# Optimization experiments

Measured on AMD Instinct MI355X. Metric: run time of the kernel, lower is better.

Reference implementation:

```python
import jax, jax.numpy as jnp
import numpy as np

N, DEG, D, L = 20000, 32, 128, 2
EPS = 1e-7
MAX_TANH_ARG = 1.0 - 1e-5


def _logmap0(x, sqrt_c):
    # Poincare ball log map at the origin: artanh(sqrt(c)||x||) * x / (sqrt(c)||x||)
    norm = jnp.maximum(jnp.linalg.norm(x, axis=-1, keepdims=True), EPS)
    arg = jnp.minimum(sqrt_c * norm, MAX_TANH_ARG)
    return jnp.arctanh(arg) * x / (sqrt_c * norm)


def _expmap0(v, sqrt_c):
    # Poincare ball exp map at the origin: tanh(sqrt(c)||v||) * v / (sqrt(c)||v||)
    norm = jnp.maximum(jnp.linalg.norm(v, axis=-1, keepdims=True), EPS)
    return jnp.tanh(sqrt_c * norm) * v / (sqrt_c * norm)


def setup_inputs() -> dict:
    key = jax.random.key(0)
    ks = jax.random.split(key, 7)
    neighbors = jax.random.randint(ks[0], (N, DEG), 0, N)  # fixed in-degree predecessor lists
    node_embeddings = jax.random.normal(ks[1], (N, D), dtype=jnp.float32)
    in_proj_w = jax.random.normal(ks[2], (L, 3 * D, D), dtype=jnp.float32) * 0.02
    in_proj_b = jax.random.normal(ks[3], (L, 3 * D), dtype=jnp.float32) * 0.02
    out_proj_w = jax.random.normal(ks[4], (L, D, D), dtype=jnp.float32) * 0.02
    out_proj_b = jax.random.normal(ks[5], (L, D), dtype=jnp.float32) * 0.02
    curvature = jnp.array([-1.0], dtype=jnp.float32)
    return {
        'neighbors': neighbors,
        'node_embeddings': node_embeddings,
        'curvature': curvature,
        'in_proj_w': in_proj_w,
        'in_proj_b': in_proj_b,
        'out_proj_w': out_proj_w,
        'out_proj_b': out_proj_b,
    }


def reference(neighbors, node_embeddings, curvature, in_proj_w, in_proj_b, out_proj_w, out_proj_b):
    sqrt_c = jnp.sqrt(jnp.abs(curvature[0]))
    scale = 1.0 / np.sqrt(D)  # torch MHA scales q by 1/sqrt(head_dim)
    x = node_embeddings
    for l in range(L):
        t = _logmap0(x, sqrt_c)                       # [N, d] tangent features
        Wq, Wk, Wv = in_proj_w[l, :D], in_proj_w[l, D:2 * D], in_proj_w[l, 2 * D:]
        bq, bk, bv = in_proj_b[l, :D], in_proj_b[l, D:2 * D], in_proj_b[l, 2 * D:]
        q = t @ Wq.T + bq                             # [N, d]
        k = t @ Wk.T + bk
        v = t @ Wv.T + bv
        kn = k[neighbors]                             # [N, deg, d] gather over predecessors
        vn = v[neighbors]                             # [N, deg, d]
        scores = jnp.einsum('nd,nkd->nk', q, kn) * scale
        attn = jax.nn.softmax(scores, axis=-1)        # [N, deg]
        h = jnp.einsum('nk,nkd->nd', attn, vn)        # [N, d]
        h = h @ out_proj_w[l].T + out_proj_b[l]
        x = _expmap0(h, sqrt_c)
    return x
```

## Files before the change

### kernel.cpp

```cpp
#include <hip/hip_runtime.h>

#define N_NODES 20000
#define N_PAD   20032
#define DEG 32
#define D 128
#define EPS 1e-7f
#define MAX_TANH_ARG (1.0f - 1e-5f)
#define SCORE_SCALE 0.08838834764831845f

typedef short bf16x8 __attribute__((ext_vector_type(8)));
typedef float f32x4 __attribute__((ext_vector_type(4)));

__device__ __forceinline__ float b2f(unsigned short u) {
  union { unsigned int i; float f; } x; x.i = ((unsigned int)u) << 16; return x.f;
}
__device__ __forceinline__ unsigned short f2b(float f) {
  union { float f; unsigned int i; } x; x.f = f;
  unsigned int r = x.i + 0x7FFFu + ((x.i >> 16) & 1u);
  return (unsigned short)(r >> 16);
}
__device__ __forceinline__ bool inputs_are_bf16(const void* curv) {
  return *(const unsigned short*)curv != 0;
}
__device__ __forceinline__ float read_sqrt_c(const void* c) {
  unsigned short u = *(const unsigned short*)c;
  float cv = (u == 0) ? *(const float*)c : b2f(u);
  return sqrtf(fabsf(cv));
}
__device__ __forceinline__ float atanh_fast(float x) {
  return 0.5f * __logf((1.f + x) / (1.f - x));
}
__device__ __forceinline__ float tanh_over_y(float y) {
  float e = __expf(-2.f * y);
  return (1.f - e) / ((1.f + e) * y);
}

__device__ __forceinline__ unsigned char f2fp8(float v) {
#if __has_builtin(__builtin_amdgcn_cvt_pk_fp8_f32)
  int p = __builtin_amdgcn_cvt_pk_fp8_f32(v, 0.f, 0, false);
  return (unsigned char)(p & 0xFF);
#else
  union { float f; unsigned u; } x; x.f = v;
  unsigned s = (x.u >> 31) << 7;
  float a = fminf(fabsf(v), 448.f);
  int q = (int)rintf(a * 512.f);
  if (q < 8) return (unsigned char)(s | q);
  int e; float m = frexpf(a, &e);
  int E = e - 1 + 7;
  int mi = (int)rintf(m * 16.f) - 8;
  if (mi == 8) { mi = 0; E += 1; }
  if (E > 15) { E = 15; mi = 6; }
  if (E < 1)  { return (unsigned char)(s | ((int)rintf(a * 512.f) & 7)); }
  return (unsigned char)(s | (E << 3) | mi);
#endif
}
__device__ __forceinline__ void fp8x8_decode(uint2 w, float* f) {
#if __has_builtin(__builtin_amdgcn_cvt_f32_fp8)
  f[0] = __builtin_amdgcn_cvt_f32_fp8((int)w.x, 0);
  f[1] = __builtin_amdgcn_cvt_f32_fp8((int)w.x, 1);
  f[2] = __builtin_amdgcn_cvt_f32_fp8((int)w.x, 2);
  f[3] = __builtin_amdgcn_cvt_f32_fp8((int)w.x, 3);
  f[4] = __builtin_amdgcn_cvt_f32_fp8((int)w.y, 0);
  f[5] = __builtin_amdgcn_cvt_f32_fp8((int)w.y, 1);
  f[6] = __builtin_amdgcn_cvt_f32_fp8((int)w.y, 2);
  f[7] = __builtin_amdgcn_cvt_f32_fp8((int)w.y, 3);
#else
#pragma unroll
  for (int i = 0; i < 8; i++) {
    unsigned char u = (i < 4) ? (unsigned char)(w.x >> (8 * i))
                              : (unsigned char)(w.y >> (8 * (i - 4)));
    int e = (u >> 3) & 15, m = u & 7;
    float mag = e ? ldexpf((float)(8 + m), e - 10) : ldexpf((float)m, -9);
    f[i] = (u & 0x80) ? -mag : mag;
  }
#endif
}

__global__ __launch_bounds__(256) void convert_kernel(
    const void* __restrict__ s0, unsigned short* __restrict__ d0, int n0,
    const void* __restrict__ s1, unsigned short* __restrict__ d1, int n1,
    const void* __restrict__ s2, unsigned short* __restrict__ d2, int n2,
    const void* __restrict__ s3, unsigned short* __restrict__ d3, int n3,
    const void* __restrict__ curv) {
  bool bf = inputs_are_bf16(curv);
  int total = n0 + n1 + n2 + n3;
  for (int i = blockIdx.x * 256 + threadIdx.x; i < total; i += gridDim.x * 256) {
    int idx = i;
    const void* s; unsigned short* d;
    if (idx < n0)                { s = s0; d = d0; }
    else if ((idx -= n0) < n1)   { s = s1; d = d1; }
    else if ((idx -= n1) < n2)   { s = s2; d = d2; }
    else { idx -= n2;              s = s3; d = d3; }
    d[idx] = bf ? ((const unsigned short*)s)[idx]
                : f2b(((const float*)s)[idx]);
  }
}

__global__ __launch_bounds__(256) void lqkv_kernel(
    const void* __restrict__ xin, int external,
    const unsigned short* __restrict__ W,
    const unsigned short* __restrict__ bias,
    unsigned short* __restrict__ qout,
    unsigned char* __restrict__ kout,
    unsigned char* __restrict__ vout,
    const void* __restrict__ curv) {
  __shared__ unsigned short t_lds[64 * 136];
  int lane = threadIdx.x & 63;
  int wave = threadIdx.x >> 6;
  int mbase = blockIdx.x * 64;
  bool srcbf = external && inputs_are_bf16(curv);
  float sqc = read_sqrt_c(curv);

  {
    int rl = threadIdx.x >> 3;
    int c8 = threadIdx.x & 7;
#pragma unroll
    for (int pass = 0; pass < 2; pass++) {
      int r = pass * 32 + rl;
      int m = mbase + r;
      float xv[16];
      if (m < N_NODES) {
        if (srcbf) {
          const bf16x8* xp = (const bf16x8*)((const unsigned short*)xin + (size_t)m * D + c8 * 16);
          bf16x8 u0 = xp[0], u1 = xp[1];
#pragma unroll
          for (int i = 0; i < 8; i++) { xv[i] = b2f((unsigned short)u0[i]); xv[8 + i] = b2f((unsigned short)u1[i]); }
        } else {
          const float4* xp = (const float4*)((const float*)xin + (size_t)m * D + c8 * 16);
#pragma unroll
          for (int i = 0; i < 4; i++) {
            float4 v = xp[i];
            xv[i * 4 + 0] = v.x; xv[i * 4 + 1] = v.y; xv[i * 4 + 2] = v.z; xv[i * 4 + 3] = v.w;
          }
        }
      } else {
#pragma unroll
        for (int i = 0; i < 16; i++) xv[i] = 0.f;
      }
      float ss = 0.f;
#pragma unroll
      for (int i = 0; i < 16; i++) ss += xv[i] * xv[i];
      ss += __shfl_xor(ss, 1); ss += __shfl_xor(ss, 2); ss += __shfl_xor(ss, 4);
      float norm = fmaxf(sqrtf(ss), EPS);
      float arg  = fminf(sqc * norm, MAX_TANH_ARG);
      float sfac = atanh_fast(arg) / (sqc * norm);
      bf16x8 o0, o1;
#pragma unroll
      for (int i = 0; i < 8; i++) {
        o0[i] = (short)f2b(xv[i] * sfac);
        o1[i] = (short)f2b(xv[8 + i] * sfac);
      }
      *(bf16x8*)&t_lds[r * 136 + c8 * 16]     = o0;
      *(bf16x8*)&t_lds[r * 136 + c8 * 16 + 8] = o1;
    }
  }
  __syncthreads();

  int quad = lane >> 4, l16 = lane & 15;
  int m0 = mbase + wave * 16;
  bf16x8 a[4];
#pragma unroll
  for (int kk = 0; kk < 4; kk++)
    a[kk] = *(const bf16x8*)&t_lds[(wave * 16 + l16) * 136 + quad * 8 + kk * 32];

  int nbase = blockIdx.y * 128;
  bool isq = (blockIdx.y == 0);
  unsigned char* out8 = (blockIdx.y == 1) ? kout : vout;

#pragma unroll
  for (int half = 0; half < 2; half++) {
    int n0g = nbase + half * 64;
    f32x4 acc[4];
#pragma unroll
    for (int s = 0; s < 4; s++) acc[s] = {0.f, 0.f, 0.f, 0.f};
#pragma unroll
    for (int s = 0; s < 4; s++) {
      const short* brow = (const short*)W + (size_t)(n0g + s * 16 + l16) * D + quad * 8;
#pragma unroll
      for (int kk = 0; kk < 4; kk++) {
        bf16x8 bfv = *(const bf16x8*)(brow + kk * 32);
        acc[s] = __builtin_amdgcn_mfma_f32_16x16x32_bf16(a[kk], bfv, acc[s], 0, 0, 0);
      }
    }
#pragma unroll
    for (int s = 0; s < 4; s++) {
      int ncol = half * 64 + s * 16 + l16;
      float bv = b2f(bias[nbase + ncol]);
#pragma unroll
      for (int r = 0; r < 4; r++) {
        int m = m0 + quad * 4 + r;
        if (m < N_NODES) {
          float val = acc[s][r] + bv;
          if (isq) qout[(size_t)m * D + ncol] = f2b(val);
          else     out8[(size_t)m * D + ncol] = f2fp8(val);
        }
      }
    }
  }
}

__global__ __launch_bounds__(256) void attn_kernel(
    const int* __restrict__ nbrs,
    const unsigned short* __restrict__ qb,
    const unsigned char* __restrict__ k8,
    const unsigned char* __restrict__ v8,
    unsigned short* __restrict__ hout) {
  int gid  = blockIdx.x * 256 + threadIdx.x;
  int node = gid >> 6;
  int lane = gid & 63;
  if (node >= N_NODES) return;
  int g = lane >> 4;
  int s = lane & 15;

  float qr[8];
  {
    bf16x8 qv = *(const bf16x8*)(qb + (size_t)node * D + s * 8);
#pragma unroll
    for (int i = 0; i < 8; i++) qr[i] = b2f((unsigned short)qv[i]);
  }
  int idx[8];
#pragma unroll
  for (int jj = 0; jj < 8; jj++) idx[jj] = nbrs[node * DEG + jj * 4 + g];

  uint2 kreg[8];
#pragma unroll
  for (int jj = 0; jj < 8; jj++)
    kreg[jj] = *(const uint2*)(k8 + (size_t)idx[jj] * D + s * 8);
  float sc[8];
#pragma unroll
  for (int jj = 0; jj < 8; jj++) {
    float kf[8];
    fp8x8_decode(kreg[jj], kf);
    float p = 0.f;
#pragma unroll
    for (int i = 0; i < 8; i++) p += kf[i] * qr[i];
    p += __shfl_xor(p, 1); p += __shfl_xor(p, 2);
    p += __shfl_xor(p, 4); p += __shfl_xor(p, 8);
    sc[jj] = p * SCORE_SCALE;
  }

  uint2 vreg[8];
#pragma unroll
  for (int jj = 0; jj < 8; jj++)
    vreg[jj] = *(const uint2*)(v8 + (size_t)idx[jj] * D + s * 8);

  float mx = sc[0];
#pragma unroll
  for (int jj = 1; jj < 8; jj++) mx = fmaxf(mx, sc[jj]);
  mx = fmaxf(mx, __shfl_xor(mx, 16));
  mx = fmaxf(mx, __shfl_xor(mx, 32));
  float sum = 0.f;
#pragma unroll
  for (int jj = 0; jj < 8; jj++) { sc[jj] = __expf(sc[jj] - mx); sum += sc[jj]; }
  sum += __shfl_xor(sum, 16);
  sum += __shfl_xor(sum, 32);
  float inv = 1.f / sum;

  float hv[8];
#pragma unroll
  for (int i = 0; i < 8; i++) hv[i] = 0.f;
#pragma unroll
  for (int jj = 0; jj < 8; jj++) {
    float aw = sc[jj] * inv;
    float vf[8];
    fp8x8_decode(vreg[jj], vf);
#pragma unroll
    for (int i = 0; i < 8; i++) hv[i] += aw * vf[i];
  }
#pragma unroll
  for (int i = 0; i < 8; i++) {
    hv[i] += __shfl_xor(hv[i], 16);
    hv[i] += __shfl_xor(hv[i], 32);
  }
  if (g == 0) {
    bf16x8 o;
#pragma unroll
    for (int i = 0; i < 8; i++) o[i] = (short)f2b(hv[i]);
    *(bf16x8*)(hout + (size_t)node * D + s * 8) = o;
  }
}

template <bool FINAL>
__global__ __launch_bounds__(256) void outproj_expmap_kernel(
    const short* __restrict__ h,
    const unsigned short* __restrict__ W,
    const unsigned short* __restrict__ bias,
    void* __restrict__ xout,
    const void* __restrict__ curv) {
  int wave = threadIdx.x >> 6;
  int lane = threadIdx.x & 63;
  int quad = lane >> 4;
  int l16  = lane & 15;
  int m0   = blockIdx.x * 64 + wave * 16;

  bf16x8 a[4];
  const short* arow = h + (size_t)(m0 + l16) * D + quad * 8;
#pragma unroll
  for (int kk = 0; kk < 4; kk++) a[kk] = *(const bf16x8*)(arow + kk * 32);

  f32x4 acc[8];
#pragma unroll
  for (int s = 0; s < 8; s++) acc[s] = {0.f, 0.f, 0.f, 0.f};
#pragma unroll
  for (int s = 0; s < 8; s++) {
    const short* brow = (const short*)W + (size_t)(s * 16 + l16) * D + quad * 8;
#pragma unroll
    for (int kk = 0; kk < 4; kk++) {
      bf16x8 bfv = *(const bf16x8*)(brow + kk * 32);
      acc[s] = __builtin_amdgcn_mfma_f32_16x16x32_bf16(a[kk], bfv, acc[s], 0, 0, 0);
    }
  }
#pragma unroll
  for (int s = 0; s < 8; s++) {
    float bv = b2f(bias[s * 16 + l16]);
#pragma unroll
    for (int r = 0; r < 4; r++) acc[s][r] += bv;
  }
  float sqc = read_sqrt_c(curv);
  float scal[4];
#pragma unroll
  for (int r = 0; r < 4; r++) {
    float ss = 0.f;
#pragma unroll
    for (int s = 0; s < 8; s++) ss += acc[s][r] * acc[s][r];
    ss += __shfl_xor(ss, 1); ss += __shfl_xor(ss, 2);
    ss += __shfl_xor(ss, 4); ss += __shfl_xor(ss, 8);
    float norm = fmaxf(sqrtf(ss), EPS);
    scal[r] = tanh_over_y(sqc * norm);
  }
  bool outbf = FINAL && inputs_are_bf16(curv);
#pragma unroll
  for (int r = 0; r < 4; r++) {
    int m = m0 + quad * 4 + r;
    if (m < N_NODES) {
#pragma unroll
      for (int s = 0; s < 8; s++) {
        float val = acc[s][r] * scal[r];
        int col = s * 16 + l16;
        if (FINAL) {
          if (outbf) ((unsigned short*)xout)[(size_t)m * D + col] = f2b(val);
          else       ((float*)xout)[(size_t)m * D + col] = val;
        } else {
          ((float*)xout)[(size_t)m * D + col] = val;
        }
      }
    }
  }
}

extern "C" void kernel_launch(void* const* d_in, const int* in_sizes, int n_in,
                              void* d_out, int out_size, void* d_ws, size_t ws_size,
                              hipStream_t stream) {
  const int* neighbors = (const int*)d_in[0];
  const void* node_emb = d_in[1];
  const void* curv     = d_in[2];
  const void* in_w     = d_in[3];
  const void* in_b     = d_in[4];
  const void* out_w    = d_in[5];
  const void* out_b    = d_in[6];

  char* ws = (char*)d_ws;
  size_t off = 0;
  auto alloc = [&](size_t bytes) {
    char* p = ws + off; off += (bytes + 255) & ~(size_t)255; return p;
  };
  unsigned short* q_bf = (unsigned short*)alloc((size_t)N_PAD * D * 2);
  unsigned char*  k_f8 = (unsigned char*)alloc((size_t)N_PAD * D);
  unsigned char*  v_f8 = (unsigned char*)alloc((size_t)N_PAD * D);
  unsigned short* h_bf = (unsigned short*)alloc((size_t)N_PAD * D * 2);
  float*          x1   = (float*)alloc((size_t)N_NODES * D * 4);
  const int n_inw = 2 * 384 * D, n_inb = 2 * 384, n_outw = 2 * D * D, n_outb = 2 * D;
  unsigned short* inw_bf  = (unsigned short*)alloc((size_t)n_inw * 2);
  unsigned short* inb_bf  = (unsigned short*)alloc((size_t)n_inb * 2);
  unsigned short* outw_bf = (unsigned short*)alloc((size_t)n_outw * 2);
  unsigned short* outb_bf = (unsigned short*)alloc((size_t)n_outb * 2);

  dim3 blk(256);
  int nodeBlocks = (N_NODES + 3) / 4;
  int mTiles     = (N_NODES + 63) / 64;

  convert_kernel<<<208, blk, 0, stream>>>(
      in_w, inw_bf, n_inw, in_b, inb_bf, n_inb,
      out_w, outw_bf, n_outw, out_b, outb_bf, n_outb, curv);

  for (int l = 0; l < 2; l++) {
    lqkv_kernel<<<dim3(mTiles, 3), blk, 0, stream>>>(
        (l == 0) ? node_emb : (const void*)x1, (l == 0) ? 1 : 0,
        inw_bf + (size_t)l * 384 * D, inb_bf + (size_t)l * 384,
        q_bf, k_f8, v_f8, curv);

    attn_kernel<<<nodeBlocks, blk, 0, stream>>>(neighbors, q_bf, k_f8, v_f8, h_bf);

    if (l == 0)
      outproj_expmap_kernel<false><<<mTiles, blk, 0, stream>>>(
          (const short*)h_bf, outw_bf + (size_t)l * D * D, outb_bf + (size_t)l * D,
          x1, curv);
    else
      outproj_expmap_kernel<true><<<mTiles, blk, 0, stream>>>(
          (const short*)h_bf, outw_bf + (size_t)l * D * D, outb_bf + (size_t)l * D,
          d_out, curv);
  }
}
```

Measured before the change: 184.6 us.

## Skip inter-layer expmap/logmap round trip and prefetch V gathers early

Uses the identity logmap0(expmap0(h)) = h. The first layer's output projection now writes the pre-expmap tangent vector as bf16, and the second layer's QKV projection reads it directly with no norm or artanh step. This drops the fp32 intermediate buffer, the transcendental work and an LDS staging pass. The identity stops holding once sqrt(c)·||h|| exceeds the artanh clamp point, so very large activations would behave differently. The attention kernel also issues the V gathers right after the K gathers so both sets of loads are in flight together, at the cost of more live registers.

```diff
diff --git a/kernel.cpp b/kernel.cpp
--- a/kernel.cpp
+++ b/kernel.cpp
@@ -96,8 +96,50 @@
   }
 }
 
+__device__ __forceinline__ void qkv_store(
+    int m0, int quad, int l16, int nbase, bool isq,
+    const f32x4* acc,
+    const unsigned short* bias, unsigned short* qout, unsigned char* out8) {
+#pragma unroll
+  for (int half = 0; half < 2; half++) {
+#pragma unroll
+    for (int s = 0; s < 4; s++) {
+      int ncol = half * 64 + s * 16 + l16;
+      float bv = b2f(bias[nbase + ncol]);
+#pragma unroll
+      for (int r = 0; r < 4; r++) {
+        int m = m0 + quad * 4 + r;
+        if (m < N_NODES) {
+          float val = acc[half * 4 + s][r] + bv;
+          if (isq) qout[(size_t)m * D + ncol] = f2b(val);
+          else     out8[(size_t)m * D + ncol] = f2fp8(val);
+        }
+      }
+    }
+  }
+}
+
+__device__ __forceinline__ void qkv_mfma(
+    const bf16x8* a, const unsigned short* W, int nbase, int quad, int l16,
+    f32x4* acc) {
+#pragma unroll
+  for (int half = 0; half < 2; half++) {
+    int n0g = nbase + half * 64;
+#pragma unroll
+    for (int s = 0; s < 4; s++) {
+      acc[half * 4 + s] = {0.f, 0.f, 0.f, 0.f};
+      const short* brow = (const short*)W + (size_t)(n0g + s * 16 + l16) * D + quad * 8;
+#pragma unroll
+      for (int kk = 0; kk < 4; kk++) {
+        bf16x8 bfv = *(const bf16x8*)(brow + kk * 32);
+        acc[half * 4 + s] = __builtin_amdgcn_mfma_f32_16x16x32_bf16(a[kk], bfv, acc[half * 4 + s], 0, 0, 0);
+      }
+    }
+  }
+}
+
 __global__ __launch_bounds__(256) void lqkv_kernel(
-    const void* __restrict__ xin, int external,
+    const void* __restrict__ xin,
     const unsigned short* __restrict__ W,
     const unsigned short* __restrict__ bias,
     unsigned short* __restrict__ qout,
@@ -108,7 +150,7 @@
   int lane = threadIdx.x & 63;
   int wave = threadIdx.x >> 6;
   int mbase = blockIdx.x * 64;
-  bool srcbf = external && inputs_are_bf16(curv);
+  bool srcbf = inputs_are_bf16(curv);
   float sqc = read_sqrt_c(curv);
 
   {
@@ -164,39 +206,34 @@
     a[kk] = *(const bf16x8*)&t_lds[(wave * 16 + l16) * 136 + quad * 8 + kk * 32];
 
   int nbase = blockIdx.y * 128;
-  bool isq = (blockIdx.y == 0);
-  unsigned char* out8 = (blockIdx.y == 1) ? kout : vout;
-
-#pragma unroll
-  for (int half = 0; half < 2; half++) {
-    int n0g = nbase + half * 64;
-    f32x4 acc[4];
-#pragma unroll
-    for (int s = 0; s < 4; s++) acc[s] = {0.f, 0.f, 0.f, 0.f};
-#pragma unroll
-    for (int s = 0; s < 4; s++) {
-      const short* brow = (const short*)W + (size_t)(n0g + s * 16 + l16) * D + quad * 8;
-#pragma unroll
-      for (int kk = 0; kk < 4; kk++) {
-        bf16x8 bfv = *(const bf16x8*)(brow + kk * 32);
-        acc[s] = __builtin_amdgcn_mfma_f32_16x16x32_bf16(a[kk], bfv, acc[s], 0, 0, 0);
-      }
-    }
-#pragma unroll
-    for (int s = 0; s < 4; s++) {
-      int ncol = half * 64 + s * 16 + l16;
-      float bv = b2f(bias[nbase + ncol]);
-#pragma unroll
-      for (int r = 0; r < 4; r++) {
-        int m = m0 + quad * 4 + r;
-        if (m < N_NODES) {
-          float val = acc[s][r] + bv;
-          if (isq) qout[(size_t)m * D + ncol] = f2b(val);
-          else     out8[(size_t)m * D + ncol] = f2fp8(val);
-        }
-      }
-    }
-  }
+  f32x4 acc[8];
+  qkv_mfma(a, W, nbase, quad, l16, acc);
+  qkv_store(m0, quad, l16, nbase, blockIdx.y == 0, acc, bias,
+            qout, (blockIdx.y == 1) ? kout : vout);
+}
+
+__global__ __launch_bounds__(256) void qkv_direct_kernel(
+    const unsigned short* __restrict__ t,
+    const unsigned short* __restrict__ W,
+    const unsigned short* __restrict__ bias,
+    unsigned short* __restrict__ qout,
+    unsigned char* __restrict__ kout,
+    unsigned char* __restrict__ vout) {
+  int lane = threadIdx.x & 63;
+  int wave = threadIdx.x >> 6;
+  int quad = lane >> 4, l16 = lane & 15;
+  int m0 = blockIdx.x * 64 + wave * 16;
+
+  bf16x8 a[4];
+  const short* arow = (const short*)t + (size_t)(m0 + l16) * D + quad * 8;
+#pragma unroll
+  for (int kk = 0; kk < 4; kk++) a[kk] = *(const bf16x8*)(arow + kk * 32);
+
+  int nbase = blockIdx.y * 128;
+  f32x4 acc[8];
+  qkv_mfma(a, W, nbase, quad, l16, acc);
+  qkv_store(m0, quad, l16, nbase, blockIdx.y == 0, acc, bias,
+            qout, (blockIdx.y == 1) ? kout : vout);
 }
 
 __global__ __launch_bounds__(256) void attn_kernel(
@@ -222,10 +259,14 @@
 #pragma unroll
   for (int jj = 0; jj < 8; jj++) idx[jj] = nbrs[node * DEG + jj * 4 + g];
 
-  uint2 kreg[8];
+  uint2 kreg[8], vreg[8];
 #pragma unroll
   for (int jj = 0; jj < 8; jj++)
     kreg[jj] = *(const uint2*)(k8 + (size_t)idx[jj] * D + s * 8);
+#pragma unroll
+  for (int jj = 0; jj < 8; jj++)
+    vreg[jj] = *(const uint2*)(v8 + (size_t)idx[jj] * D + s * 8);
+
   float sc[8];
 #pragma unroll
   for (int jj = 0; jj < 8; jj++) {
@@ -239,11 +280,6 @@
     sc[jj] = p * SCORE_SCALE;
   }
 
-  uint2 vreg[8];
-#pragma unroll
-  for (int jj = 0; jj < 8; jj++)
-    vreg[jj] = *(const uint2*)(v8 + (size_t)idx[jj] * D + s * 8);
-
   float mx = sc[0];
 #pragma unroll
   for (int jj = 1; jj < 8; jj++) mx = fmaxf(mx, sc[jj]);
@@ -280,8 +316,8 @@
   }
 }
 
-template <bool FINAL>
-__global__ __launch_bounds__(256) void outproj_expmap_kernel(
+template <int MODE>
+__global__ __launch_bounds__(256) void outproj_kernel(
     const short* __restrict__ h,
     const unsigned short* __restrict__ W,
     const unsigned short* __restrict__ bias,
@@ -316,32 +352,34 @@
 #pragma unroll
     for (int r = 0; r < 4; r++) acc[s][r] += bv;
   }
-  float sqc = read_sqrt_c(curv);
   float scal[4];
-#pragma unroll
-  for (int r = 0; r < 4; r++) {
-    float ss = 0.f;
-#pragma unroll
-    for (int s = 0; s < 8; s++) ss += acc[s][r] * acc[s][r];
-    ss += __shfl_xor(ss, 1); ss += __shfl_xor(ss, 2);
-    ss += __shfl_xor(ss, 4); ss += __shfl_xor(ss, 8);
-    float norm = fmaxf(sqrtf(ss), EPS);
-    scal[r] = tanh_over_y(sqc * norm);
-  }
-  bool outbf = FINAL && inputs_are_bf16(curv);
+  if (MODE == 1) {
+    float sqc = read_sqrt_c(curv);
+#pragma unroll
+    for (int r = 0; r < 4; r++) {
+      float ss = 0.f;
+#pragma unroll
+      for (int s = 0; s < 8; s++) ss += acc[s][r] * acc[s][r];
+      ss += __shfl_xor(ss, 1); ss += __shfl_xor(ss, 2);
+      ss += __shfl_xor(ss, 4); ss += __shfl_xor(ss, 8);
+      float norm = fmaxf(sqrtf(ss), EPS);
+      scal[r] = tanh_over_y(sqc * norm);
+    }
+  }
+  bool outbf = (MODE == 1) && inputs_are_bf16(curv);
 #pragma unroll
   for (int r = 0; r < 4; r++) {
     int m = m0 + quad * 4 + r;
     if (m < N_NODES) {
 #pragma unroll
       for (int s = 0; s < 8; s++) {
-        float val = acc[s][r] * scal[r];
         int col = s * 16 + l16;
-        if (FINAL) {
+        if (MODE == 0) {
+          ((unsigned short*)xout)[(size_t)m * D + col] = f2b(acc[s][r]);
+        } else {
+          float val = acc[s][r] * scal[r];
           if (outbf) ((unsigned short*)xout)[(size_t)m * D + col] = f2b(val);
           else       ((float*)xout)[(size_t)m * D + col] = val;
-        } else {
-          ((float*)xout)[(size_t)m * D + col] = val;
         }
       }
     }
@@ -368,7 +406,7 @@
   unsigned char*  k_f8 = (unsigned char*)alloc((size_t)N_PAD * D);
   unsigned char*  v_f8 = (unsigned char*)alloc((size_t)N_PAD * D);
   unsigned short* h_bf = (unsigned short*)alloc((size_t)N_PAD * D * 2);
-  float*          x1   = (float*)alloc((size_t)N_NODES * D * 4);
+  unsigned short* t1_bf = (unsigned short*)alloc((size_t)N_PAD * D * 2);
   const int n_inw = 2 * 384 * D, n_inb = 2 * 384, n_outw = 2 * D * D, n_outb = 2 * D;
   unsigned short* inw_bf  = (unsigned short*)alloc((size_t)n_inw * 2);
   unsigned short* inb_bf  = (unsigned short*)alloc((size_t)n_inb * 2);
@@ -383,21 +421,15 @@
       in_w, inw_bf, n_inw, in_b, inb_bf, n_inb,
       out_w, outw_bf, n_outw, out_b, outb_bf, n_outb, curv);
 
-  for (int l = 0; l < 2; l++) {
-    lqkv_kernel<<<dim3(mTiles, 3), blk, 0, stream>>>(
-        (l == 0) ? node_emb : (const void*)x1, (l == 0) ? 1 : 0,
-        inw_bf + (size_t)l * 384 * D, inb_bf + (size_t)l * 384,
-        q_bf, k_f8, v_f8, curv);
-
-    attn_kernel<<<nodeBlocks, blk, 0, stream>>>(neighbors, q_bf, k_f8, v_f8, h_bf);
-
-    if (l == 0)
-      outproj_expmap_kernel<false><<<mTiles, blk, 0, stream>>>(
-          (const short*)h_bf, outw_bf + (size_t)l * D * D, outb_bf + (size_t)l * D,
-          x1, curv);
-    else
-      outproj_expmap_kernel<true><<<mTiles, blk, 0, stream>>>(
-          (const short*)h_bf, outw_bf + (size_t)l * D * D, outb_bf + (size_t)l * D,
-          d_out, curv);
-  }
-}
+  lqkv_kernel<<<dim3(mTiles, 3), blk, 0, stream>>>(
+      node_emb, inw_bf, inb_bf, q_bf, k_f8, v_f8, curv);
+  attn_kernel<<<nodeBlocks, blk, 0, stream>>>(neighbors, q_bf, k_f8, v_f8, h_bf);
+  outproj_kernel<0><<<mTiles, blk, 0, stream>>>(
+      (const short*)h_bf, outw_bf, outb_bf, t1_bf, curv);
+
+  qkv_direct_kernel<<<dim3(mTiles, 3), blk, 0, stream>>>(
+      t1_bf, inw_bf + (size_t)384 * D, inb_bf + 384, q_bf, k_f8, v_f8);
+  attn_kernel<<<nodeBlocks, blk, 0, stream>>>(neighbors, q_bf, k_f8, v_f8, h_bf);
+  outproj_kernel<1><<<mTiles, blk, 0, stream>>>(
+      (const short*)h_bf, outw_bf + (size_t)D * D, outb_bf + D, d_out, curv);
+}
```

New measurement: 184.5 us. No clear change (-0.1%).
